# Kernel tuning notes

Hardware: AMD Instinct MI355X
Metric: run time of the kernel (lower is better)

The kernel has to match this reference:

```python
import jax, jax.numpy as jnp
import numpy as np

N, D, B, C, T, TOD = 8192, 32, 2, 8, 12, 288
PARAM_SCALE = 0.3  # keep relu+softmax logits well-conditioned (original uses plain randn init)


def setup_inputs() -> dict:
    key = jax.random.key(0)
    k0, k1, k2, k3, k4 = jax.random.split(key, 5)
    return {
        "x": jax.random.normal(k0, (B, C, N, T), dtype=jnp.float32),
        "nodevec1": PARAM_SCALE * jax.random.normal(k1, (N, D), dtype=jnp.float32),
        "nodevec2": PARAM_SCALE * jax.random.normal(k2, (N, D), dtype=jnp.float32),
        "timevec": PARAM_SCALE * jax.random.normal(k3, (TOD, D), dtype=jnp.float32),
        "k": PARAM_SCALE * jax.random.normal(k4, (D, D, D), dtype=jnp.float32),
        "time_ind": 100,
    }


def reference(x, nodevec1, nodevec2, timevec, k, time_ind):
    # Dynamic Tucker-decomposition adjacency (SpatialGraphConv.forward, eval mode -> dropout is identity)
    tv = timevec[time_ind]                             # [D]   time_vec
    core = jnp.einsum('d,def->ef', tv, k)              # [D,D] adp1 (squeezed)
    # adp2/adp3 chain: (nodevec1 @ core) @ nodevec2.T  -> [N,N]
    adp = jnp.einsum('ne,ef->nf', nodevec1, core)      # [N,D]
    adp = jnp.einsum('nf,mf->nm', adp, nodevec2)       # [N,N]
    adp = jax.nn.softmax(jax.nn.relu(adp), axis=-1)    # row-softmax over neighbors
    # NConv: neighbor aggregation  'bcnt,nm->bcmt'
    return jnp.einsum('bcnt,nm->bcmt', x, adp)
```

## Files before the change

### kernel.cpp

```cpp
#include <hip/hip_runtime.h>
#include <hip/hip_bf16.h>


#define NN 8192
#define DD 32
#define TT 12
#define NSPLIT 8
#define CHUNK 1024

typedef __attribute__((ext_vector_type(8))) short bf16x8;
typedef __attribute__((ext_vector_type(4))) float f32x4;

static __device__ __forceinline__ unsigned short f2bf(float f) {
  unsigned int u = __float_as_uint(f);
  u = (u + 0x7FFFu + ((u >> 16) & 1u)) >> 16;
  return (unsigned short)u;
}

static __device__ __forceinline__ float fexp2(float x) {
#if __has_builtin(__builtin_amdgcn_exp2f)
  return __builtin_amdgcn_exp2f(x);
#else
  return __builtin_exp2f(x);
#endif
}

#define MFMA32(A, B, C) __builtin_amdgcn_mfma_f32_16x16x32_bf16((A), (B), (C), 0, 0, 0)

__global__ __launch_bounds__(256) void k_prep(const float* __restrict__ nv1,
                                              const float* __restrict__ nv2,
                                              const float* __restrict__ timevec,
                                              const float* __restrict__ kk,
                                              const int* __restrict__ tind,
                                              unsigned short* __restrict__ t1b,
                                              unsigned short* __restrict__ nv2b,
                                              float* __restrict__ sums) {
  __shared__ float cs[1024];
  const int tid = threadIdx.x;
  if (tid < 128) sums[blockIdx.x * 128 + tid] = 0.f;
  const float* tv = timevec + (size_t)tind[0] * DD;
  for (int idx = tid; idx < 1024; idx += 256) {
    float acc = 0.f;
#pragma unroll
    for (int d = 0; d < DD; ++d) acc += tv[d] * kk[d * 1024 + idx];
    cs[idx] = acc;
  }
  __syncthreads();
  const int nbase = blockIdx.x * 128;
  const int f = tid & 31, sub = tid >> 5;
#pragma unroll 4
  for (int it = 0; it < 16; ++it) {
    const int n = nbase + it * 8 + sub;
    const float* nr = nv1 + (size_t)n * DD;
    float acc = 0.f;
#pragma unroll
    for (int e = 0; e < DD; ++e) acc += nr[e] * cs[e * DD + f];
    t1b[(size_t)n * DD + f] = f2bf(acc * 1.4426950408889634f);
  }
#pragma unroll 4
  for (int it = 0; it < 16; ++it) {
    const int idx = nbase * DD + it * 256 + tid;
    nv2b[idx] = f2bf(nv2[idx]);
  }
}

__global__ __launch_bounds__(256) void k_stats(const unsigned short* __restrict__ t1b,
                                               const unsigned short* __restrict__ nv2b,
                                               float* __restrict__ sums) {
  const int tid = threadIdx.x;
  const int w = tid >> 6, lane = tid & 63, q = lane >> 4, i16 = lane & 15;
  const int nbase = blockIdx.x * 64 + w * 16;
  bf16x8 a = *(const bf16x8*)(t1b + (size_t)(nbase + i16) * DD + q * 8);
  const f32x4 z4 = {0.f, 0.f, 0.f, 0.f};
  float s[4] = {0.f, 0.f, 0.f, 0.f};
  const int m0 = blockIdx.y * 1024;
  for (int mt = m0; mt < m0 + 1024; mt += 64) {
#pragma unroll
    for (int u = 0; u < 4; ++u) {
      bf16x8 b = *(const bf16x8*)(nv2b + (size_t)(mt + u * 16 + i16) * DD + q * 8);
      f32x4 d = __builtin_amdgcn_mfma_f32_16x16x32_bf16(a, b, z4, 0, 0, 0);
#pragma unroll
      for (int r = 0; r < 4; ++r) s[r] += fexp2(fmaxf(d[r], 0.f));
    }
  }
#pragma unroll
  for (int r = 0; r < 4; ++r)
    for (int off = 1; off < 16; off <<= 1) s[r] += __shfl_xor(s[r], off, 64);
  if (i16 == 0) {
#pragma unroll
    for (int r = 0; r < 4; ++r) atomicAdd(&sums[nbase + q * 4 + r], s[r]);
  }
}

__global__ __launch_bounds__(256) void k_y(const float* __restrict__ x,
                                           const float* __restrict__ sums,
                                           unsigned short* __restrict__ yT) {
  __shared__ float xs[3328];
  const int tid = threadIdx.x;
  const int n0 = blockIdx.x * 256;
  const int bc = blockIdx.y;
  const float* xp = x + (size_t)bc * NN * TT + (size_t)n0 * TT;
#pragma unroll
  for (int j = 0; j < 12; ++j) {
    const int idx = j * 256 + tid;
    xs[(idx / 12) * 13 + idx % 12] = xp[idx];
  }
  __syncthreads();
  const float rinv = 1.0f / sums[n0 + tid];
#pragma unroll
  for (int t = 0; t < 12; ++t)
    yT[(size_t)(bc * TT + t) * NN + n0 + tid] = f2bf(xs[tid * 13 + t] * rinv);
}

__global__ __launch_bounds__(256) void k_mega(const unsigned short* __restrict__ t1b,
                                              const unsigned short* __restrict__ nv2b,
                                              const unsigned short* __restrict__ yT,
                                              float* __restrict__ part) {
  const int tid = threadIdx.x;
  const int w = tid >> 6, lane = tid & 63, q = lane >> 4, i16 = lane & 15;
  const int mb = blockIdx.x * 64;
  const int nt0 = blockIdx.y * CHUNK;

  bf16x8 bg[4];
#pragma unroll
  for (int ms = 0; ms < 4; ++ms)
    bg[ms] = *(const bf16x8*)(nv2b + (size_t)(mb + ms * 16 + i16) * DD + q * 8);

  f32x4 acc[3][4];
#pragma unroll
  for (int c = 0; c < 3; ++c)
#pragma unroll
    for (int ms = 0; ms < 4; ++ms) acc[c][ms] = (f32x4){0.f, 0.f, 0.f, 0.f};

  const int perm = ((i16 >> 2) << 3) | (i16 & 3);
  const unsigned short* tp = t1b + (size_t)(nt0 + perm) * DD + q * 8;
  const unsigned short* yp0 = yT + (size_t)((w * 3 + 0) * 16 + i16) * NN + nt0 + q * 8;
  const unsigned short* yp1 = yp0 + (size_t)16 * NN;
  const unsigned short* yp2 = yp1 + (size_t)16 * NN;

  bf16x8 alo = *(const bf16x8*)tp;
  bf16x8 ahi = *(const bf16x8*)(tp + 4 * DD);
  bf16x8 y0 = *(const bf16x8*)yp0;
  bf16x8 y1 = *(const bf16x8*)yp1;
  bf16x8 y2 = *(const bf16x8*)yp2;

  const f32x4 z4 = {0.f, 0.f, 0.f, 0.f};

  for (int sl = 0; sl < 32; ++sl) {
    bf16x8 alo_n, ahi_n, y0n, y1n, y2n;
    if (sl < 31) {
      const int o = (sl + 1) * 32;
      alo_n = *(const bf16x8*)(tp + o * DD);
      ahi_n = *(const bf16x8*)(tp + o * DD + 4 * DD);
      y0n = *(const bf16x8*)(yp0 + o);
      y1n = *(const bf16x8*)(yp1 + o);
      y2n = *(const bf16x8*)(yp2 + o);
    } else {
      alo_n = alo; ahi_n = ahi; y0n = y0; y1n = y1; y2n = y2;
    }

    bf16x8 e[4];
#pragma unroll
    for (int ms = 0; ms < 4; ++ms) {
      f32x4 dlo = MFMA32(alo, bg[ms], z4);
      f32x4 dhi = MFMA32(ahi, bg[ms], z4);
      bf16x8 t;
#pragma unroll
      for (int r = 0; r < 4; ++r) {
        t[r] = (short)f2bf(fexp2(fmaxf(dlo[r], 0.f)));
        t[4 + r] = (short)f2bf(fexp2(fmaxf(dhi[r], 0.f)));
      }
      e[ms] = t;
    }

#pragma unroll
    for (int ms = 0; ms < 4; ++ms) {
      acc[0][ms] = MFMA32(y0, e[ms], acc[0][ms]);
      acc[1][ms] = MFMA32(y1, e[ms], acc[1][ms]);
      acc[2][ms] = MFMA32(y2, e[ms], acc[2][ms]);
    }

    alo = alo_n; ahi = ahi_n; y0 = y0n; y1 = y1n; y2 = y2n;
  }

  float* pp = part + (size_t)blockIdx.y * 192 * NN;
#pragma unroll
  for (int c = 0; c < 3; ++c)
#pragma unroll
    for (int ms = 0; ms < 4; ++ms) {
      const int colbase = (w * 3 + c) * 16 + q * 4;
      const int m = mb + ms * 16 + i16;
#pragma unroll
      for (int r = 0; r < 4; ++r)
        pp[(size_t)(colbase + r) * NN + m] = acc[c][ms][r];
    }
}

__global__ __launch_bounds__(256) void k_reduce(const float* __restrict__ part,
                                                float* __restrict__ out) {
  __shared__ float os[3328];
  const int tid = threadIdx.x;
  const int m0 = blockIdx.x * 256;
  const int bc = blockIdx.y;
#pragma unroll
  for (int t = 0; t < 12; ++t) {
    const int col = bc * TT + t;
    float s = 0.f;
#pragma unroll
    for (int nc = 0; nc < NSPLIT; ++nc)
      s += part[((size_t)nc * 192 + col) * NN + m0 + tid];
    os[tid * 13 + t] = s;
  }
  __syncthreads();
  float* op = out + (size_t)bc * NN * TT + (size_t)m0 * TT;
#pragma unroll
  for (int j = 0; j < 12; ++j) {
    const int idx = j * 256 + tid;
    op[idx] = os[(idx / 12) * 13 + idx % 12];
  }
}

extern "C" void kernel_launch(void* const* d_in, const int* in_sizes, int n_in,
                              void* d_out, int out_size, void* d_ws, size_t ws_size,
                              hipStream_t stream) {
  const float* x = (const float*)d_in[0];
  const float* nv1 = (const float*)d_in[1];
  const float* nv2 = (const float*)d_in[2];
  const float* tv = (const float*)d_in[3];
  const float* kk = (const float*)d_in[4];
  const int* tind = (const int*)d_in[5];
  float* out = (float*)d_out;

  char* ws = (char*)d_ws;
  unsigned short* t1b  = (unsigned short*)(ws);
  unsigned short* nv2b = (unsigned short*)(ws + 524288);
  float* sums          = (float*)(ws + 1048576);
  unsigned short* yT   = (unsigned short*)(ws + 1081344);
  float* part          = (float*)(ws + 4227072);

  k_prep<<<64, 256, 0, stream>>>(nv1, nv2, tv, kk, tind, t1b, nv2b, sums);
  k_stats<<<dim3(128, 8), 256, 0, stream>>>(t1b, nv2b, sums);
  k_y<<<dim3(32, 16), 256, 0, stream>>>(x, sums, yT);
  k_mega<<<dim3(128, NSPLIT), 256, 0, stream>>>(t1b, nv2b, yT, part);
  k_reduce<<<dim3(32, 16), 256, 0, stream>>>(part, out);
}
```

Measured before the change: 193.1 us.

## Software-pipeline exp-score MFMAs against aggregation MFMAs in k_mega

Restructures the k_mega main loop so the score MFMAs and relu/exp2/bf16 packing for the next slice are interleaved with the aggregation MFMAs of the current slice. This lets matrix and vector work overlap instead of serializing within each iteration, with a prologue and epilogue to fill and drain the pipeline. It also packs bf16 conversions two at a time into 32-bit words and sets a minimum-occupancy hint of 3 blocks. The extra live registers could cause spills under the new occupancy bound.

```diff
diff --git a/kernel.cpp b/kernel.cpp
--- a/kernel.cpp
+++ b/kernel.cpp
@@ -10,6 +10,7 @@
 
 typedef __attribute__((ext_vector_type(8))) short bf16x8;
 typedef __attribute__((ext_vector_type(4))) float f32x4;
+typedef __attribute__((ext_vector_type(4))) unsigned int u32x4;
 
 static __device__ __forceinline__ unsigned short f2bf(float f) {
   unsigned int u = __float_as_uint(f);
@@ -26,6 +27,23 @@
 }
 
 #define MFMA32(A, B, C) __builtin_amdgcn_mfma_f32_16x16x32_bf16((A), (B), (C), 0, 0, 0)
+
+static __device__ __forceinline__ unsigned int pk_rne(float a, float b) {
+  unsigned int ua = __float_as_uint(a);
+  unsigned int ub = __float_as_uint(b);
+  ua = ua + 0x7FFFu + ((ua >> 16) & 1u);
+  ub = ub + 0x7FFFu + ((ub >> 16) & 1u);
+  return (ua >> 16) | (ub & 0xFFFF0000u);
+}
+
+static __device__ __forceinline__ bf16x8 relu_exp2_pack(f32x4 lo, f32x4 hi) {
+  u32x4 t;
+  t[0] = pk_rne(fexp2(fmaxf(lo[0], 0.f)), fexp2(fmaxf(lo[1], 0.f)));
+  t[1] = pk_rne(fexp2(fmaxf(lo[2], 0.f)), fexp2(fmaxf(lo[3], 0.f)));
+  t[2] = pk_rne(fexp2(fmaxf(hi[0], 0.f)), fexp2(fmaxf(hi[1], 0.f)));
+  t[3] = pk_rne(fexp2(fmaxf(hi[2], 0.f)), fexp2(fmaxf(hi[3], 0.f)));
+  return __builtin_bit_cast(bf16x8, t);
+}
 
 __global__ __launch_bounds__(256) void k_prep(const float* __restrict__ nv1,
                                               const float* __restrict__ nv2,
@@ -112,10 +130,10 @@
     yT[(size_t)(bc * TT + t) * NN + n0 + tid] = f2bf(xs[tid * 13 + t] * rinv);
 }
 
-__global__ __launch_bounds__(256) void k_mega(const unsigned short* __restrict__ t1b,
-                                              const unsigned short* __restrict__ nv2b,
-                                              const unsigned short* __restrict__ yT,
-                                              float* __restrict__ part) {
+__global__ __launch_bounds__(256, 3) void k_mega(const unsigned short* __restrict__ t1b,
+                                                 const unsigned short* __restrict__ nv2b,
+                                                 const unsigned short* __restrict__ yT,
+                                                 float* __restrict__ part) {
   const int tid = threadIdx.x;
   const int w = tid >> 6, lane = tid & 63, q = lane >> 4, i16 = lane & 15;
   const int mb = blockIdx.x * 64;
@@ -138,49 +156,66 @@
   const unsigned short* yp1 = yp0 + (size_t)16 * NN;
   const unsigned short* yp2 = yp1 + (size_t)16 * NN;
 
+  const f32x4 z4 = {0.f, 0.f, 0.f, 0.f};
+
   bf16x8 alo = *(const bf16x8*)tp;
   bf16x8 ahi = *(const bf16x8*)(tp + 4 * DD);
+  bf16x8 e[4];
+#pragma unroll
+  for (int ms = 0; ms < 4; ++ms) {
+    f32x4 dlo = MFMA32(alo, bg[ms], z4);
+    f32x4 dhi = MFMA32(ahi, bg[ms], z4);
+    e[ms] = relu_exp2_pack(dlo, dhi);
+  }
   bf16x8 y0 = *(const bf16x8*)yp0;
   bf16x8 y1 = *(const bf16x8*)yp1;
   bf16x8 y2 = *(const bf16x8*)yp2;
-
-  const f32x4 z4 = {0.f, 0.f, 0.f, 0.f};
-
-  for (int sl = 0; sl < 32; ++sl) {
-    bf16x8 alo_n, ahi_n, y0n, y1n, y2n;
-    if (sl < 31) {
-      const int o = (sl + 1) * 32;
-      alo_n = *(const bf16x8*)(tp + o * DD);
-      ahi_n = *(const bf16x8*)(tp + o * DD + 4 * DD);
-      y0n = *(const bf16x8*)(yp0 + o);
-      y1n = *(const bf16x8*)(yp1 + o);
-      y2n = *(const bf16x8*)(yp2 + o);
-    } else {
-      alo_n = alo; ahi_n = ahi; y0n = y0; y1n = y1; y2n = y2;
-    }
-
-    bf16x8 e[4];
-#pragma unroll
-    for (int ms = 0; ms < 4; ++ms) {
-      f32x4 dlo = MFMA32(alo, bg[ms], z4);
-      f32x4 dhi = MFMA32(ahi, bg[ms], z4);
-      bf16x8 t;
-#pragma unroll
-      for (int r = 0; r < 4; ++r) {
-        t[r] = (short)f2bf(fexp2(fmaxf(dlo[r], 0.f)));
-        t[4 + r] = (short)f2bf(fexp2(fmaxf(dhi[r], 0.f)));
-      }
-      e[ms] = t;
-    }
-
-#pragma unroll
-    for (int ms = 0; ms < 4; ++ms) {
-      acc[0][ms] = MFMA32(y0, e[ms], acc[0][ms]);
-      acc[1][ms] = MFMA32(y1, e[ms], acc[1][ms]);
-      acc[2][ms] = MFMA32(y2, e[ms], acc[2][ms]);
-    }
-
-    alo = alo_n; ahi = ahi_n; y0 = y0n; y1 = y1n; y2 = y2n;
+  alo = *(const bf16x8*)(tp + 32 * DD);
+  ahi = *(const bf16x8*)(tp + 36 * DD);
+
+  for (int sl = 1; sl < 32; ++sl) {
+    const int o = sl * 32;
+    bf16x8 y0n = *(const bf16x8*)(yp0 + o);
+    bf16x8 y1n = *(const bf16x8*)(yp1 + o);
+    bf16x8 y2n = *(const bf16x8*)(yp2 + o);
+    bf16x8 alo_n = *(const bf16x8*)(tp + (size_t)(o + 32) * DD);
+    bf16x8 ahi_n = *(const bf16x8*)(tp + (size_t)(o + 36) * DD);
+
+    f32x4 d00 = MFMA32(alo, bg[0], z4);
+    f32x4 d01 = MFMA32(ahi, bg[0], z4);
+    f32x4 d10 = MFMA32(alo, bg[1], z4);
+    f32x4 d11 = MFMA32(ahi, bg[1], z4);
+    acc[0][0] = MFMA32(y0, e[0], acc[0][0]);
+    acc[1][0] = MFMA32(y1, e[0], acc[1][0]);
+    acc[2][0] = MFMA32(y2, e[0], acc[2][0]);
+    acc[0][1] = MFMA32(y0, e[1], acc[0][1]);
+    acc[1][1] = MFMA32(y1, e[1], acc[1][1]);
+    acc[2][1] = MFMA32(y2, e[1], acc[2][1]);
+    e[0] = relu_exp2_pack(d00, d01);
+    e[1] = relu_exp2_pack(d10, d11);
+
+    f32x4 d20 = MFMA32(alo, bg[2], z4);
+    f32x4 d21 = MFMA32(ahi, bg[2], z4);
+    f32x4 d30 = MFMA32(alo, bg[3], z4);
+    f32x4 d31 = MFMA32(ahi, bg[3], z4);
+    acc[0][2] = MFMA32(y0, e[2], acc[0][2]);
+    acc[1][2] = MFMA32(y1, e[2], acc[1][2]);
+    acc[2][2] = MFMA32(y2, e[2], acc[2][2]);
+    acc[0][3] = MFMA32(y0, e[3], acc[0][3]);
+    acc[1][3] = MFMA32(y1, e[3], acc[1][3]);
+    acc[2][3] = MFMA32(y2, e[3], acc[2][3]);
+    e[2] = relu_exp2_pack(d20, d21);
+    e[3] = relu_exp2_pack(d30, d31);
+
+    y0 = y0n; y1 = y1n; y2 = y2n;
+    alo = alo_n; ahi = ahi_n;
+  }
+
+#pragma unroll
+  for (int ms = 0; ms < 4; ++ms) {
+    acc[0][ms] = MFMA32(y0, e[ms], acc[0][ms]);
+    acc[1][ms] = MFMA32(y1, e[ms], acc[1][ms]);
+    acc[2][ms] = MFMA32(y2, e[ms], acc[2][ms]);
   }
 
   float* pp = part + (size_t)blockIdx.y * 192 * NN;
```

After: 184.3 us. 1.05x faster.
